# Kernel optimization log

Measured on AMD Instinct MI355X. Metric: run time of the kernel, lower is better.

## Reference

```python
import jax, jax.numpy as jnp
import numpy as np

B, C, H, W = 16, 512, 64, 64
K = 4            # num_experts
D = C // 16      # reduction=16 -> hidden channels 32


def setup_inputs() -> dict:
    key = jax.random.key(0)
    ks = jax.random.split(key, 7)
    s_fc = 1.0 / np.sqrt(C)
    s_w1 = 1.0 / np.sqrt(C)   # conv1x1 fan_in = C
    s_w2 = 1.0 / np.sqrt(D)   # conv1x1 fan_in = D
    return {
        "x": jax.random.normal(ks[0], (B, C, H, W), dtype=jnp.float32),
        "fc_w": jax.random.uniform(ks[1], (K, C), minval=-s_fc, maxval=s_fc, dtype=jnp.float32),
        "fc_b": jax.random.uniform(ks[2], (K,), minval=-s_fc, maxval=s_fc, dtype=jnp.float32),
        "w1": jax.random.uniform(ks[3], (K, D, C), minval=-s_w1, maxval=s_w1, dtype=jnp.float32),
        "b1": jax.random.uniform(ks[4], (K, D), minval=-s_w1, maxval=s_w1, dtype=jnp.float32),
        "w2": jax.random.uniform(ks[5], (K, C, D), minval=-s_w2, maxval=s_w2, dtype=jnp.float32),
        "b2": jax.random.uniform(ks[6], (K, C), minval=-s_w2, maxval=s_w2, dtype=jnp.float32),
    }


def reference(x, fc_w, fc_b, w1, b1, w2, b2):
    # global average pool -> routing weights over K experts
    y = jnp.mean(x, axis=(2, 3))                                  # [B, C]
    weights = jax.nn.softmax(y @ fc_w.T + fc_b, axis=1)           # [B, K]
    # all experts' first conv1x1 + ReLU, batched over K
    hid = jax.nn.relu(
        jnp.einsum("bchw,kdc->bkdhw", x, w1) + b1[None, :, :, None, None]
    )                                                             # [B, K, D, H, W]
    # second conv1x1 fused with the weighted sum over experts (avoids [B,K,C,H,W])
    out = jnp.einsum("bkdhw,kcd,bk->bchw", hid, w2, weights)
    out = out + jnp.einsum("bk,kc->bc", weights, b2)[:, :, None, None]
    attn = jax.nn.sigmoid(out)                                    # [B, C, H, W]
    return x * attn
```

## Files before the change

### kernel.cpp

```cpp
#include <hip/hip_runtime.h>
#include <hip/hip_bf16.h>
#include <math.h>

#define BB 16
#define CC 512
#define HWN 4096
#define KK 4
#define DD 32
#define KD 128
#define NPIX 64

typedef __attribute__((ext_vector_type(8))) short short8;
typedef __attribute__((ext_vector_type(4))) float f32x4;

#define WS_Y     0
#define WS_WGT   8192
#define WS_BIAS2 8256
#define WS_W1B   16448
#define WS_W2B   49216

__device__ inline unsigned short f2bf(float f) {
    unsigned u = __builtin_bit_cast(unsigned, f);
    unsigned r = (u + 0x7FFFu + ((u >> 16) & 1u)) >> 16;
    return (unsigned short)r;
}

__global__ __launch_bounds__(256) void mean_kernel(const float* __restrict__ x,
                                                   float* __restrict__ y) {
    int wave = threadIdx.x >> 6;
    int lane = threadIdx.x & 63;
    int row  = blockIdx.x * 4 + wave;
    const float4* xr = (const float4*)(x + (size_t)row * HWN);
    float s = 0.f;
    #pragma unroll
    for (int i = 0; i < 16; i++) {
        float4 v = xr[i * 64 + lane];
        s += (v.x + v.y) + (v.z + v.w);
    }
    #pragma unroll
    for (int off = 32; off > 0; off >>= 1)
        s += __shfl_down(s, off, 64);
    if (lane == 0) y[row] = s * (1.0f / HWN);
}

__global__ __launch_bounds__(64) void route_kernel(const float* __restrict__ y,
                                                   const float* __restrict__ fc_w,
                                                   const float* __restrict__ fc_b,
                                                   float* __restrict__ wgt) {
    __shared__ float logits[BB][KK];
    int t = threadIdx.x;
    int b = t >> 2, k = t & 3;
    const float4* y4 = (const float4*)(y + b * CC);
    const float4* f4 = (const float4*)(fc_w + k * CC);
    float s = fc_b[k];
    for (int i = 0; i < CC / 4; i++) {
        float4 a = y4[i], w = f4[i];
        s += a.x * w.x + a.y * w.y + a.z * w.z + a.w * w.w;
    }
    logits[b][k] = s;
    __syncthreads();
    if (k == 0) {
        float m = logits[b][0];
        #pragma unroll
        for (int j = 1; j < KK; j++) m = fmaxf(m, logits[b][j]);
        float e[KK], sum = 0.f;
        #pragma unroll
        for (int j = 0; j < KK; j++) { e[j] = __expf(logits[b][j] - m); sum += e[j]; }
        float inv = 1.f / sum;
        #pragma unroll
        for (int j = 0; j < KK; j++) wgt[b * KK + j] = e[j] * inv;
    }
}

__global__ __launch_bounds__(256) void prep_kernel(const float* __restrict__ w1,
                                                   const float* __restrict__ w2,
                                                   const float* __restrict__ b2,
                                                   const float* __restrict__ wgt,
                                                   unsigned short* __restrict__ w1b,
                                                   unsigned short* __restrict__ w2b,
                                                   float* __restrict__ bias2) {
    int tid = blockIdx.x * 256 + threadIdx.x;
    int n   = gridDim.x * 256;
    for (int idx = tid; idx < CC * KD; idx += n) {
        int f = idx >> 9, rem = idx & 511;
        int l = rem >> 3, i = rem & 7;
        int ks = f >> 3, m = f & 7;
        int kd = m * 16 + (l & 15);
        int c  = ks * 32 + (l >> 4) * 8 + i;
        w1b[idx] = f2bf(w1[kd * CC + c]);
    }
    for (int idx = tid; idx < CC * KD; idx += n) {
        int f = idx >> 9, rem = idx & 511;
        int l = rem >> 3, i = rem & 7;
        int mc = f >> 2, kk = f & 3;
        int c = mc * 16 + (l & 15);
        int d = (l >> 4) * 8 + i;
        w2b[idx] = f2bf(w2[(kk * CC + c) * DD + d]);
    }
    for (int idx = tid; idx < BB * CC; idx += n) {
        int bb = idx >> 9, c = idx & 511;
        float s = 0.f;
        #pragma unroll
        for (int k = 0; k < KK; k++) s += wgt[bb * KK + k] * b2[k * CC + c];
        bias2[idx] = s;
    }
}

__global__ __launch_bounds__(256, 2) void main_kernel(const float* __restrict__ x,
                                                      const unsigned short* __restrict__ w1b,
                                                      const float* __restrict__ b1,
                                                      const unsigned short* __restrict__ w2b,
                                                      const float* __restrict__ wgt,
                                                      const float* __restrict__ bias2,
                                                      float* __restrict__ out) {
    __shared__ unsigned short hid_lds[NPIX * KD];

    const int b       = blockIdx.y;
    const int pixbase = blockIdx.x * NPIX;
    const int tid = threadIdx.x;
    const int wv  = tid >> 6;
    const int l   = tid & 63;
    const int l15 = l & 15, lg = l >> 4;

    const float* xb = x + (size_t)b * CC * HWN;
    const short8* w1f = (const short8*)w1b;
    const short8* w2f = (const short8*)w2b;

    f32x4 acc1[8];
    #pragma unroll
    for (int m = 0; m < 8; m++) acc1[m] = (f32x4)0.f;

    const int mypix = pixbase + wv * 16 + l15;
    #pragma unroll 2
    for (int ks = 0; ks < 16; ks++) {
        const float* xcol = xb + (size_t)(ks * 32 + lg * 8) * HWN + mypix;
        short8 bf;
        #pragma unroll
        for (int i = 0; i < 8; i++) bf[i] = (short)f2bf(xcol[(size_t)i * HWN]);
        #pragma unroll
        for (int m = 0; m < 8; m++) {
            short8 af = w1f[(ks * 8 + m) * 64 + l];
            acc1[m] = __builtin_amdgcn_mfma_f32_16x16x32_bf16(af, bf, acc1[m], 0, 0, 0);
        }
    }

    {
        const int row = wv * 16 + l15;
        #pragma unroll
        for (int m = 0; m < 8; m++) {
            f32x4 bv = *(const f32x4*)(b1 + m * 16 + lg * 4);
            float w = wgt[b * KK + (m >> 1)];
            unsigned short h[4];
            #pragma unroll
            for (int r = 0; r < 4; r++) {
                float t = fmaxf(acc1[m][r] + bv[r], 0.f) * w;
                h[r] = f2bf(t);
            }
            unsigned lo = (unsigned)h[0] | ((unsigned)h[1] << 16);
            unsigned hi = (unsigned)h[2] | ((unsigned)h[3] << 16);
            int byteoff = row * 256 + (m * 16 + lg * 4) * 2;
            byteoff ^= (row & 7) << 4;
            uint2 v; v.x = lo; v.y = hi;
            *(uint2*)((char*)hid_lds + byteoff) = v;
        }
    }
    __syncthreads();

    short8 breg[4][4];
    #pragma unroll
    for (int kk = 0; kk < 4; kk++) {
        #pragma unroll
        for (int nb = 0; nb < 4; nb++) {
            int row = nb * 16 + l15;
            int byteoff = row * 256 + (kk * 32 + lg * 8) * 2;
            byteoff ^= (row & 7) << 4;
            breg[kk][nb] = *(const short8*)((const char*)hid_lds + byteoff);
        }
    }

    const int wcbase = wv * 128;
    #pragma unroll 2
    for (int mblk = 0; mblk < 8; mblk++) {
        f32x4 acc[4];
        #pragma unroll
        for (int nb = 0; nb < 4; nb++) acc[nb] = (f32x4)0.f;
        #pragma unroll
        for (int kk = 0; kk < 4; kk++) {
            short8 af = w2f[((wv * 8 + mblk) * 4 + kk) * 64 + l];
            #pragma unroll
            for (int nb = 0; nb < 4; nb++)
                acc[nb] = __builtin_amdgcn_mfma_f32_16x16x32_bf16(af, breg[kk][nb], acc[nb], 0, 0, 0);
        }
        const int cb = wcbase + mblk * 16 + lg * 4;
        f32x4 b2v = *(const f32x4*)(bias2 + b * CC + cb);
        #pragma unroll
        for (int nb = 0; nb < 4; nb++) {
            int pix = pixbase + nb * 16 + l15;
            #pragma unroll
            for (int r = 0; r < 4; r++) {
                size_t off = ((size_t)b * CC + cb + r) * HWN + pix;
                float s = acc[nb][r] + b2v[r];
                float attn = __builtin_amdgcn_rcpf(1.f + __expf(-s));
                out[off] = x[off] * attn;
            }
        }
    }
}

extern "C" void kernel_launch(void* const* d_in, const int* in_sizes, int n_in,
                              void* d_out, int out_size, void* d_ws, size_t ws_size,
                              hipStream_t stream) {
    const float* x    = (const float*)d_in[0];
    const float* fc_w = (const float*)d_in[1];
    const float* fc_b = (const float*)d_in[2];
    const float* w1   = (const float*)d_in[3];
    const float* b1   = (const float*)d_in[4];
    const float* w2   = (const float*)d_in[5];
    const float* b2   = (const float*)d_in[6];
    float* out = (float*)d_out;
    float* ws  = (float*)d_ws;

    float* y     = ws + WS_Y;
    float* wgt   = ws + WS_WGT;
    float* bias2 = ws + WS_BIAS2;
    unsigned short* w1b = (unsigned short*)(ws + WS_W1B);
    unsigned short* w2b = (unsigned short*)(ws + WS_W2B);

    mean_kernel <<<dim3(BB * CC / 4), dim3(256), 0, stream>>>(x, y);
    route_kernel<<<dim3(1),           dim3(64),  0, stream>>>(y, fc_w, fc_b, wgt);
    prep_kernel <<<dim3(128),         dim3(256), 0, stream>>>(w1, w2, b2, wgt, w1b, w2b, bias2);
    main_kernel <<<dim3(HWN / NPIX, BB), dim3(256), 0, stream>>>(x, w1b, b1, w2b, wgt, bias2, out);
}
```

Measured before the change: 334.4 us.

## Split main kernel's channel reduction across 8 waves with LDS partial-sum combine

```diff
diff --git a/kernel.cpp b/kernel.cpp
--- a/kernel.cpp
+++ b/kernel.cpp
@@ -106,14 +106,14 @@
     }
 }
 
-__global__ __launch_bounds__(256, 2) void main_kernel(const float* __restrict__ x,
+__global__ __launch_bounds__(512, 4) void main_kernel(const float* __restrict__ x,
                                                       const unsigned short* __restrict__ w1b,
                                                       const float* __restrict__ b1,
                                                       const unsigned short* __restrict__ w2b,
                                                       const float* __restrict__ wgt,
                                                       const float* __restrict__ bias2,
                                                       float* __restrict__ out) {
-    __shared__ unsigned short hid_lds[NPIX * KD];
+    __shared__ char lds[4 * 8192];
 
     const int b       = blockIdx.y;
     const int pixbase = blockIdx.x * NPIX;
@@ -121,6 +121,8 @@
     const int wv  = tid >> 6;
     const int l   = tid & 63;
     const int l15 = l & 15, lg = l >> 4;
+    const int pg  = wv & 3;
+    const int kh  = wv >> 2;
 
     const float* xb = x + (size_t)b * CC * HWN;
     const short8* w1f = (const short8*)w1b;
@@ -130,13 +132,24 @@
     #pragma unroll
     for (int m = 0; m < 8; m++) acc1[m] = (f32x4)0.f;
 
-    const int mypix = pixbase + wv * 16 + l15;
-    #pragma unroll 2
-    for (int ks = 0; ks < 16; ks++) {
-        const float* xcol = xb + (size_t)(ks * 32 + lg * 8) * HWN + mypix;
+    const int mypix = pixbase + pg * 16 + l15;
+    const float* xc = xb + (size_t)(kh * 256 + lg * 8) * HWN + mypix;
+
+    float xv[8];
+    #pragma unroll
+    for (int i = 0; i < 8; i++) xv[i] = xc[(size_t)i * HWN];
+
+    #pragma unroll
+    for (int ks8 = 0; ks8 < 8; ks8++) {
         short8 bf;
         #pragma unroll
-        for (int i = 0; i < 8; i++) bf[i] = (short)f2bf(xcol[(size_t)i * HWN]);
+        for (int i = 0; i < 8; i++) bf[i] = (short)f2bf(xv[i]);
+        if (ks8 < 7) {
+            const float* xn = xc + (size_t)((ks8 + 1) * 32) * HWN;
+            #pragma unroll
+            for (int i = 0; i < 8; i++) xv[i] = xn[(size_t)i * HWN];
+        }
+        const int ks = kh * 8 + ks8;
         #pragma unroll
         for (int m = 0; m < 8; m++) {
             short8 af = w1f[(ks * 8 + m) * 64 + l];
@@ -144,55 +157,64 @@
         }
     }
 
-    {
-        const int row = wv * 16 + l15;
-        #pragma unroll
-        for (int m = 0; m < 8; m++) {
-            f32x4 bv = *(const f32x4*)(b1 + m * 16 + lg * 4);
-            float w = wgt[b * KK + (m >> 1)];
-            unsigned short h[4];
-            #pragma unroll
-            for (int r = 0; r < 4; r++) {
-                float t = fmaxf(acc1[m][r] + bv[r], 0.f) * w;
-                h[r] = f2bf(t);
+    if (kh == 1) {
+        char* base = lds + pg * 8192 + lg * 256 + l15 * 16;
+        #pragma unroll
+        for (int m = 0; m < 8; m++)
+            *(f32x4*)(base + m * 1024) = acc1[m];
+    }
+    __syncthreads();
+
+    if (kh == 0) {
+        const char* pbase = lds + pg * 8192 + lg * 256 + l15 * 16;
+        #pragma unroll
+        for (int half = 0; half < 2; half++) {
+            f32x4 pp[4];
+            #pragma unroll
+            for (int m4 = 0; m4 < 4; m4++)
+                pp[m4] = *(const f32x4*)(pbase + (half * 4 + m4) * 1024);
+            #pragma unroll
+            for (int m4 = 0; m4 < 4; m4++) {
+                const int m = half * 4 + m4;
+                f32x4 bv = *(const f32x4*)(b1 + m * 16 + lg * 4);
+                float wk = wgt[b * KK + (m >> 1)];
+                f32x4 s = acc1[m] + pp[m4];
+                unsigned short h[4];
+                #pragma unroll
+                for (int r = 0; r < 4; r++) {
+                    float t = fmaxf(s[r] + bv[r], 0.f) * wk;
+                    h[r] = f2bf(t);
+                }
+                unsigned lo = (unsigned)h[0] | ((unsigned)h[1] << 16);
+                unsigned hi = (unsigned)h[2] | ((unsigned)h[3] << 16);
+                int byteoff = pg * 8192 + l15 * 256 + (m * 16 + lg * 4) * 2;
+                byteoff ^= (l15 & 7) << 4;
+                uint2 v; v.x = lo; v.y = hi;
+                *(uint2*)(lds + byteoff) = v;
             }
-            unsigned lo = (unsigned)h[0] | ((unsigned)h[1] << 16);
-            unsigned hi = (unsigned)h[2] | ((unsigned)h[3] << 16);
-            int byteoff = row * 256 + (m * 16 + lg * 4) * 2;
-            byteoff ^= (row & 7) << 4;
-            uint2 v; v.x = lo; v.y = hi;
-            *(uint2*)((char*)hid_lds + byteoff) = v;
         }
     }
     __syncthreads();
 
-    short8 breg[4][4];
-    #pragma unroll
-    for (int kk = 0; kk < 4; kk++) {
-        #pragma unroll
-        for (int nb = 0; nb < 4; nb++) {
-            int row = nb * 16 + l15;
-            int byteoff = row * 256 + (kk * 32 + lg * 8) * 2;
-            byteoff ^= (row & 7) << 4;
-            breg[kk][nb] = *(const short8*)((const char*)hid_lds + byteoff);
-        }
-    }
-
-    const int wcbase = wv * 128;
-    #pragma unroll 2
-    for (int mblk = 0; mblk < 8; mblk++) {
+    const float* bb2 = bias2 + b * CC;
+    #pragma unroll
+    for (int mblk = 0; mblk < 4; mblk++) {
         f32x4 acc[4];
         #pragma unroll
         for (int nb = 0; nb < 4; nb++) acc[nb] = (f32x4)0.f;
         #pragma unroll
         for (int kk = 0; kk < 4; kk++) {
-            short8 af = w2f[((wv * 8 + mblk) * 4 + kk) * 64 + l];
-            #pragma unroll
-            for (int nb = 0; nb < 4; nb++)
-                acc[nb] = __builtin_amdgcn_mfma_f32_16x16x32_bf16(af, breg[kk][nb], acc[nb], 0, 0, 0);
-        }
-        const int cb = wcbase + mblk * 16 + lg * 4;
-        f32x4 b2v = *(const f32x4*)(bias2 + b * CC + cb);
+            short8 af = w2f[((wv * 4 + mblk) * 4 + kk) * 64 + l];
+            #pragma unroll
+            for (int nb = 0; nb < 4; nb++) {
+                int byteoff = nb * 8192 + l15 * 256 + kk * 64 + lg * 16;
+                byteoff ^= (l15 & 7) << 4;
+                short8 bf = *(const short8*)(lds + byteoff);
+                acc[nb] = __builtin_amdgcn_mfma_f32_16x16x32_bf16(af, bf, acc[nb], 0, 0, 0);
+            }
+        }
+        const int cb = wv * 64 + mblk * 16 + lg * 4;
+        f32x4 b2v = *(const f32x4*)(bb2 + cb);
         #pragma unroll
         for (int nb = 0; nb < 4; nb++) {
             int pix = pixbase + nb * 16 + l15;
@@ -201,7 +223,7 @@
                 size_t off = ((size_t)b * CC + cb + r) * HWN + pix;
                 float s = acc[nb][r] + b2v[r];
                 float attn = __builtin_amdgcn_rcpf(1.f + __expf(-s));
-                out[off] = x[off] * attn;
+                __builtin_nontemporal_store(x[off] * attn, &out[off]);
             }
         }
     }
@@ -229,5 +251,5 @@
     mean_kernel <<<dim3(BB * CC / 4), dim3(256), 0, stream>>>(x, y);
     route_kernel<<<dim3(1),           dim3(64),  0, stream>>>(y, fc_w, fc_b, wgt);
     prep_kernel <<<dim3(128),         dim3(256), 0, stream>>>(w1, w2, b2, wgt, w1b, w2b, bias2);
-    main_kernel <<<dim3(HWN / NPIX, BB), dim3(256), 0, stream>>>(x, w1b, b1, w2b, wgt, bias2, out);
-}
+    main_kernel <<<dim3(HWN / NPIX, BB), dim3(512), 0, stream>>>(x, w1b, b1, w2b, wgt, bias2, out);
+}
```

New measurement: 307.6 us. -8.0%, faster.

## Give each wave an independent 16-pixel job and exchange hidden activations via shuffles

Applied to the files above, without the earlier changes.

```diff
diff --git a/kernel.cpp b/kernel.cpp
--- a/kernel.cpp
+++ b/kernel.cpp
@@ -8,7 +8,6 @@
 #define KK 4
 #define DD 32
 #define KD 128
-#define NPIX 64
 
 typedef __attribute__((ext_vector_type(8))) short short8;
 typedef __attribute__((ext_vector_type(4))) float f32x4;
@@ -106,23 +105,22 @@
     }
 }
 
-__global__ __launch_bounds__(256, 2) void main_kernel(const float* __restrict__ x,
+__global__ __launch_bounds__(256, 4) void main_kernel(const float* __restrict__ x,
                                                       const unsigned short* __restrict__ w1b,
                                                       const float* __restrict__ b1,
                                                       const unsigned short* __restrict__ w2b,
                                                       const float* __restrict__ wgt,
                                                       const float* __restrict__ bias2,
                                                       float* __restrict__ out) {
-    __shared__ unsigned short hid_lds[NPIX * KD];
-
-    const int b       = blockIdx.y;
-    const int pixbase = blockIdx.x * NPIX;
     const int tid = threadIdx.x;
     const int wv  = tid >> 6;
     const int l   = tid & 63;
     const int l15 = l & 15, lg = l >> 4;
-
-    const float* xb = x + (size_t)b * CC * HWN;
+    const int job = blockIdx.x * 4 + wv;
+    const int b   = job >> 8;
+    const int px  = ((job & 255) << 4) + l15;
+
+    const float* xb = x + (size_t)b * CC * HWN + px;
     const short8* w1f = (const short8*)w1b;
     const short8* w2f = (const short8*)w2b;
 
@@ -130,13 +128,20 @@
     #pragma unroll
     for (int m = 0; m < 8; m++) acc1[m] = (f32x4)0.f;
 
-    const int mypix = pixbase + wv * 16 + l15;
-    #pragma unroll 2
+    float xv[8];
+    #pragma unroll
+    for (int i = 0; i < 8; i++) xv[i] = xb[(size_t)(lg * 8 + i) * HWN];
+
+    #pragma unroll
     for (int ks = 0; ks < 16; ks++) {
-        const float* xcol = xb + (size_t)(ks * 32 + lg * 8) * HWN + mypix;
         short8 bf;
         #pragma unroll
-        for (int i = 0; i < 8; i++) bf[i] = (short)f2bf(xcol[(size_t)i * HWN]);
+        for (int i = 0; i < 8; i++) bf[i] = (short)f2bf(xv[i]);
+        if (ks < 15) {
+            const float* xn = xb + (size_t)((ks + 1) * 32 + lg * 8) * HWN;
+            #pragma unroll
+            for (int i = 0; i < 8; i++) xv[i] = xn[(size_t)i * HWN];
+        }
         #pragma unroll
         for (int m = 0; m < 8; m++) {
             short8 af = w1f[(ks * 8 + m) * 64 + l];
@@ -144,65 +149,57 @@
         }
     }
 
-    {
-        const int row = wv * 16 + l15;
-        #pragma unroll
-        for (int m = 0; m < 8; m++) {
-            f32x4 bv = *(const f32x4*)(b1 + m * 16 + lg * 4);
-            float w = wgt[b * KK + (m >> 1)];
-            unsigned short h[4];
-            #pragma unroll
-            for (int r = 0; r < 4; r++) {
-                float t = fmaxf(acc1[m][r] + bv[r], 0.f) * w;
-                h[r] = f2bf(t);
-            }
-            unsigned lo = (unsigned)h[0] | ((unsigned)h[1] << 16);
-            unsigned hi = (unsigned)h[2] | ((unsigned)h[3] << 16);
-            int byteoff = row * 256 + (m * 16 + lg * 4) * 2;
-            byteoff ^= (row & 7) << 4;
-            uint2 v; v.x = lo; v.y = hi;
-            *(uint2*)((char*)hid_lds + byteoff) = v;
-        }
-    }
-    __syncthreads();
-
-    short8 breg[4][4];
+    unsigned hp[16];
+    #pragma unroll
+    for (int m = 0; m < 8; m++) {
+        f32x4 bv = *(const f32x4*)(b1 + m * 16 + lg * 4);
+        float wk = wgt[b * KK + (m >> 1)];
+        unsigned short h[4];
+        #pragma unroll
+        for (int r = 0; r < 4; r++)
+            h[r] = f2bf(fmaxf(acc1[m][r] + bv[r], 0.f) * wk);
+        hp[m * 2 + 0] = (unsigned)h[0] | ((unsigned)h[1] << 16);
+        hp[m * 2 + 1] = (unsigned)h[2] | ((unsigned)h[3] << 16);
+    }
+
+    const int src0 = l15 + 16 * ((lg & 1) * 2 + 0);
+    const int src1 = l15 + 16 * ((lg & 1) * 2 + 1);
+    const bool hi = ((lg >> 1) & 1) != 0;
+    unsigned bw[4][4];
+    #pragma unroll
+    for (int m = 0; m < 8; m++) {
+        const bool take = (((m & 1) != 0) == hi);
+        #pragma unroll
+        for (int rp = 0; rp < 2; rp++) {
+            int v0 = __shfl((int)hp[m * 2 + rp], src0, 64);
+            int v1 = __shfl((int)hp[m * 2 + rp], src1, 64);
+            if (take) { bw[m >> 1][rp] = (unsigned)v0; bw[m >> 1][rp + 2] = (unsigned)v1; }
+        }
+    }
+    short8 breg[4];
     #pragma unroll
     for (int kk = 0; kk < 4; kk++) {
-        #pragma unroll
-        for (int nb = 0; nb < 4; nb++) {
-            int row = nb * 16 + l15;
-            int byteoff = row * 256 + (kk * 32 + lg * 8) * 2;
-            byteoff ^= (row & 7) << 4;
-            breg[kk][nb] = *(const short8*)((const char*)hid_lds + byteoff);
-        }
-    }
-
-    const int wcbase = wv * 128;
-    #pragma unroll 2
-    for (int mblk = 0; mblk < 8; mblk++) {
-        f32x4 acc[4];
-        #pragma unroll
-        for (int nb = 0; nb < 4; nb++) acc[nb] = (f32x4)0.f;
+        uint4 u; u.x = bw[kk][0]; u.y = bw[kk][1]; u.z = bw[kk][2]; u.w = bw[kk][3];
+        breg[kk] = __builtin_bit_cast(short8, u);
+    }
+
+    const float* bb2 = bias2 + b * CC;
+    #pragma unroll 4
+    for (int mblk = 0; mblk < 32; mblk++) {
+        f32x4 acc = (f32x4)0.f;
         #pragma unroll
         for (int kk = 0; kk < 4; kk++) {
-            short8 af = w2f[((wv * 8 + mblk) * 4 + kk) * 64 + l];
-            #pragma unroll
-            for (int nb = 0; nb < 4; nb++)
-                acc[nb] = __builtin_amdgcn_mfma_f32_16x16x32_bf16(af, breg[kk][nb], acc[nb], 0, 0, 0);
-        }
-        const int cb = wcbase + mblk * 16 + lg * 4;
-        f32x4 b2v = *(const f32x4*)(bias2 + b * CC + cb);
-        #pragma unroll
-        for (int nb = 0; nb < 4; nb++) {
-            int pix = pixbase + nb * 16 + l15;
-            #pragma unroll
-            for (int r = 0; r < 4; r++) {
-                size_t off = ((size_t)b * CC + cb + r) * HWN + pix;
-                float s = acc[nb][r] + b2v[r];
-                float attn = __builtin_amdgcn_rcpf(1.f + __expf(-s));
-                out[off] = x[off] * attn;
-            }
+            short8 af = w2f[(mblk * 4 + kk) * 64 + l];
+            acc = __builtin_amdgcn_mfma_f32_16x16x32_bf16(af, breg[kk], acc, 0, 0, 0);
+        }
+        const int cb = mblk * 16 + lg * 4;
+        f32x4 b2v = *(const f32x4*)(bb2 + cb);
+        #pragma unroll
+        for (int r = 0; r < 4; r++) {
+            size_t off = ((size_t)b * CC + cb + r) * HWN + px;
+            float s = acc[r] + b2v[r];
+            float attn = __builtin_amdgcn_rcpf(1.f + __expf(-s));
+            __builtin_nontemporal_store(x[off] * attn, &out[off]);
         }
     }
 }
@@ -229,5 +226,5 @@
     mean_kernel <<<dim3(BB * CC / 4), dim3(256), 0, stream>>>(x, y);
     route_kernel<<<dim3(1),           dim3(64),  0, stream>>>(y, fc_w, fc_b, wgt);
     prep_kernel <<<dim3(128),         dim3(256), 0, stream>>>(w1, w2, b2, wgt, w1b, w2b, bias2);
-    main_kernel <<<dim3(HWN / NPIX, BB), dim3(256), 0, stream>>>(x, w1b, b1, w2b, wgt, bias2, out);
-}
+    main_kernel <<<dim3(4096 / 4),    dim3(256), 0, stream>>>(x, w1b, b1, w2b, wgt, bias2, out);
+}
```

Measured after the change: 331.0 us. About the same (-1.0%).
